# Kernel tuning notes

Measured on AMD Instinct MI355X. Metric: run time of the kernel, lower is better.

## Reference

```python
import jax, jax.numpy as jnp
import numpy as np

DROP_P = 0.5
DROP_KEY = jax.random.key(42)  # fixed key: deterministic dropout mask


def setup_inputs() -> dict:
    key = jax.random.key(0)
    k1, k2, k3 = jax.random.split(key, 3)
    B, H, S, D = 2, 16, 2048, 128
    x1 = jax.random.normal(k1, (B, H, S, D), dtype=jnp.float32)
    x2 = jax.random.normal(k2, (B, H, S, D), dtype=jnp.float32)
    # broadcastable per-head divisor; offset to keep it away from zero
    x3 = jax.random.uniform(k3, (B, H, 1, 1), dtype=jnp.float32) + 1.0
    return {"x1": x1, "x2": x2, "x3": x3}


def reference(x1, x2, x3):
    # v1 = x1 @ x2^T  -> [B,H,S,S]; v2 = v1 / x3 (broadcast divisor)
    scores = jnp.einsum('bhqd,bhkd->bhqk', x1, x2) / x3
    # v3 = softmax over last dim
    probs = jax.nn.softmax(scores, axis=-1)
    # v4 = dropout(p=0.5), training=True semantics: mask and rescale by 1/(1-p)
    keep = jax.random.bernoulli(DROP_KEY, 1.0 - DROP_P, probs.shape)
    probs = jnp.where(keep, probs / (1.0 - DROP_P), 0.0)
    # v5 = v4 @ x1 (note: values are x1, not a separate V); v6 = v5 + x2 residual
    out = jnp.einsum('bhqk,bhkd->bhqd', probs, x1) + x2
    return out
```

## Files before the change

### kernel.cpp

```cpp
#include <hip/hip_runtime.h>
#include <math.h>


constexpr int Sc = 2048, Dc = 128;
constexpr int BK = 64, NT = Sc / BK;
constexpr int KS_B = 16384, VS_B = 16384;
constexpr int PS_B = 8192;

typedef short bf16x8 __attribute__((ext_vector_type(8)));
typedef float f32x4 __attribute__((ext_vector_type(4)));
union U8 { uint4 u; bf16x8 v; };

__device__ __forceinline__ unsigned rotl32(unsigned x, int r) {
  return (x << r) | (x >> (32 - r));
}

__device__ __forceinline__ void tf2x32(unsigned x0, unsigned x1,
                                       unsigned &o0, unsigned &o1) {
  const unsigned ks0 = 0u, ks1 = 42u;
  const unsigned ks2 = 0x1BD11BDAu ^ 0u ^ 42u;
  x0 += ks0; x1 += ks1;
#define TFR(r) { x0 += x1; x1 = rotl32(x1, r); x1 ^= x0; }
  TFR(13) TFR(15) TFR(26) TFR(6)
  x0 += ks1; x1 += ks2 + 1u;
  TFR(17) TFR(29) TFR(16) TFR(24)
  x0 += ks2; x1 += ks0 + 2u;
  TFR(13) TFR(15) TFR(26) TFR(6)
  x0 += ks0; x1 += ks1 + 3u;
  TFR(17) TFR(29) TFR(16) TFR(24)
  x0 += ks1; x1 += ks2 + 4u;
  TFR(13) TFR(15) TFR(26) TFR(6)
  x0 += ks2; x1 += ks0 + 5u;
#undef TFR
  o0 = x0; o1 = x1;
}

__device__ __forceinline__ unsigned pk2rn(float a, float b) {
  return __builtin_amdgcn_perm(__float_as_uint(b) + 0x8000u,
                               __float_as_uint(a) + 0x8000u, 0x07060302u);
}

__device__ __forceinline__ void gload16(const void* g, void* l) {
  __builtin_amdgcn_global_load_lds(
      (const __attribute__((address_space(1))) void*)g,
      (__attribute__((address_space(3))) void*)l, 16, 0, 0);
}

__global__ __launch_bounds__(256)
void prepack(const float* __restrict__ x1, const float* __restrict__ x2,
             uint4* __restrict__ Kb, uint4* __restrict__ Vt) {
  __shared__ ushort Vl[64 * 68];
  const int tid = threadIdx.x, blk = blockIdx.x;
  const int half = blk & 1, tile = blk >> 1;
  const float* x2t = x2 + (size_t)tile * 8192;
  const float* x1t = x1 + (size_t)tile * 8192;
  uint4* KbT = Kb + (size_t)tile * 1024;
  uint4* VtT = Vt + (size_t)tile * 1024;
#pragma unroll
  for (int it = 0; it < 2; ++it) {
    int u = half * 512 + it * 256 + tid;
    int mt = u >> 8, c = (u >> 6) & 3, g = (u >> 4) & 3, m16 = u & 15;
    const float4* s = (const float4*)(x2t + (mt * 16 + m16) * 128 + c * 32 + g * 8);
    float4 f0 = s[0], f1 = s[1];
    KbT[u] = uint4{pk2rn(f0.x, f0.y), pk2rn(f0.z, f0.w),
                   pk2rn(f1.x, f1.y), pk2rn(f1.z, f1.w)};
  }
#pragma unroll
  for (int it = 0; it < 4; ++it) {
    int f = it * 256 + tid;
    int row = f >> 4, c4 = f & 15;
    float4 v = *(const float4*)(x1t + row * 128 + half * 64 + c4 * 4);
    *(uint2*)&Vl[row * 68 + c4 * 4] = uint2{pk2rn(v.x, v.y), pk2rn(v.z, v.w)};
  }
  __syncthreads();
#pragma unroll
  for (int it = 0; it < 2; ++it) {
    int ul = it * 256 + tid;
    int dtl = ul >> 7, c = (ul >> 6) & 1, g = (ul >> 4) & 3, m16 = ul & 15;
    int dl = dtl * 16 + m16, k0 = c * 32 + g * 8;
    unsigned w[4];
#pragma unroll
    for (int p = 0; p < 4; ++p) {
      unsigned lo = Vl[(k0 + 2 * p) * 68 + dl];
      unsigned hi = Vl[(k0 + 2 * p + 1) * 68 + dl];
      w[p] = lo | (hi << 16);
    }
    VtT[(((dtl + half * 4) * 2 + c) * 4 + g) * 16 + m16] = uint4{w[0], w[1], w[2], w[3]};
  }
}

__global__ __launch_bounds__(256, 4)
void attn4(const uint4* __restrict__ Kb, const uint4* __restrict__ Vt,
           const float* __restrict__ x1, const float* __restrict__ x2,
           const float* __restrict__ x3, float* __restrict__ out) {
  __shared__ uint4 smemv[(KS_B + VS_B + PS_B) / 16];
  char* smem = (char*)smemv;
  ushort* Ps = (ushort*)(smem + KS_B + VS_B);
  float* Os = (float*)smem;

  const int tid = threadIdx.x, wave = tid >> 6, lane = tid & 63;
  const int g = lane >> 4, q = lane & 15;
  const int blk = blockIdx.x, bh = blk & 31, qt = blk >> 5;

  const float* X1 = x1 + (size_t)bh * (Sc * Dc);
  const float* X2 = x2 + (size_t)bh * (Sc * Dc);
  float* outp = out + (size_t)bh * (Sc * Dc);
  const float cl2 = (1.0f / x3[bh]) * 1.4426950408889634f;

  const int qrow = qt * 64 + wave * 16 + q;
  const unsigned row_base = (unsigned)(bh * Sc + qrow) * (unsigned)Sc;

  bf16x8 qf[4];
  {
    const float4* qsrc = (const float4*)(X1 + (size_t)qrow * Dc);
#pragma unroll
    for (int c = 0; c < 4; ++c) {
      float4 f0 = qsrc[c * 8 + g * 2], f1 = qsrc[c * 8 + g * 2 + 1];
      U8 cv; cv.u = uint4{pk2rn(f0.x, f0.y), pk2rn(f0.z, f0.w),
                          pk2rn(f1.x, f1.y), pk2rn(f1.z, f1.w)};
      qf[c] = cv.v;
    }
  }

  f32x4 o[8];
#pragma unroll
  for (int i = 0; i < 8; ++i) o[i] = f32x4{0.f, 0.f, 0.f, 0.f};
  float l_run = 0.0f;
  const int tbase = bh * 32;
  ushort* pw = Ps + wave * 1024 + q * 64;

  for (int t = 0; t < NT; ++t) {
    __syncthreads();
    {
      const char* kg = (const char*)(Kb + (size_t)(tbase + t) * 1024);
      const char* vg = (const char*)(Vt + (size_t)(tbase + t) * 1024);
#pragma unroll
      for (int j = 0; j < 4; ++j) {
        int off = j * 4096 + wave * 1024 + lane * 16;
        gload16(kg + off, smem + off);
        gload16(vg + off, smem + KS_B + off);
      }
    }
    __syncthreads();

    f32x4 s0 = {}, s1 = {}, s2 = {}, s3 = {};
#pragma unroll
    for (int c = 0; c < 4; ++c) {
      U8 a0; a0.u = *(const uint4*)(smem + ((0 * 4 + c) * 64 + lane) * 16);
      U8 a1; a1.u = *(const uint4*)(smem + ((1 * 4 + c) * 64 + lane) * 16);
      U8 a2; a2.u = *(const uint4*)(smem + ((2 * 4 + c) * 64 + lane) * 16);
      U8 a3; a3.u = *(const uint4*)(smem + ((3 * 4 + c) * 64 + lane) * 16);
      s0 = __builtin_amdgcn_mfma_f32_16x16x32_bf16(a0.v, qf[c], s0, 0, 0, 0);
      s1 = __builtin_amdgcn_mfma_f32_16x16x32_bf16(a1.v, qf[c], s1, 0, 0, 0);
      s2 = __builtin_amdgcn_mfma_f32_16x16x32_bf16(a2.v, qf[c], s2, 0, 0, 0);
      s3 = __builtin_amdgcn_mfma_f32_16x16x32_bf16(a3.v, qf[c], s3, 0, 0, 0);
    }

    float pr[16];
    float ls = 0.0f;
#pragma unroll
    for (int i = 0; i < 4; ++i) { pr[i]      = __builtin_amdgcn_exp2f(s0[i] * cl2); ls += pr[i]; }
#pragma unroll
    for (int i = 0; i < 4; ++i) { pr[4 + i]  = __builtin_amdgcn_exp2f(s1[i] * cl2); ls += pr[4 + i]; }
#pragma unroll
    for (int i = 0; i < 4; ++i) { pr[8 + i]  = __builtin_amdgcn_exp2f(s2[i] * cl2); ls += pr[8 + i]; }
#pragma unroll
    for (int i = 0; i < 4; ++i) { pr[12 + i] = __builtin_amdgcn_exp2f(s3[i] * cl2); ls += pr[12 + i]; }
    ls += __shfl_xor(ls, 16);
    ls += __shfl_xor(ls, 32);
    l_run += ls;

    unsigned db = 0u;
    {
      const unsigned ib = row_base + (unsigned)(t * 64) + (unsigned)(g * 4);
#pragma unroll 4
      for (unsigned j = 0; j < 16; ++j) {
        unsigned key = ((j & 12u) << 2) | (j & 3u);
        unsigned a, b;
        tf2x32(0u, ib + key, a, b);
        db |= ((a ^ b) >> 31) << j;
      }
    }

#pragma unroll
    for (int mt = 0; mt < 4; ++mt) {
      float a0_ = ((db >> (mt * 4 + 0)) & 1u) ? 0.f : pr[mt * 4 + 0];
      float a1_ = ((db >> (mt * 4 + 1)) & 1u) ? 0.f : pr[mt * 4 + 1];
      float a2_ = ((db >> (mt * 4 + 2)) & 1u) ? 0.f : pr[mt * 4 + 2];
      float a3_ = ((db >> (mt * 4 + 3)) & 1u) ? 0.f : pr[mt * 4 + 3];
      *(uint2*)&pw[((mt * 4 + g) ^ q) * 4] = uint2{pk2rn(a0_, a1_), pk2rn(a2_, a3_)};
    }

#pragma unroll
    for (int c2 = 0; c2 < 2; ++c2) {
      int u0 = c2 * 8 + g * 2;
      uint2 b0 = *(const uint2*)&pw[(u0 ^ q) * 4];
      uint2 b1 = *(const uint2*)&pw[((u0 + 1) ^ q) * 4];
      U8 bfr; bfr.u = uint4{b0.x, b0.y, b1.x, b1.y};
#pragma unroll
      for (int dt = 0; dt < 8; ++dt) {
        U8 av; av.u = *(const uint4*)(smem + KS_B + ((dt * 2 + c2) * 64 + lane) * 16);
        o[dt] = __builtin_amdgcn_mfma_f32_16x16x32_bf16(av.v, bfr.v, o[dt], 0, 0, 0);
      }
    }
  }

  const float invl = 2.0f / l_run;
  __syncthreads();
  {
    float* ow = Os + (size_t)(wave * 16 + q) * 132;
#pragma unroll
    for (int dt = 0; dt < 8; ++dt) {
      int d = dt * 16 + g * 4;
      *(float4*)&ow[d] = float4{o[dt][0] * invl, o[dt][1] * invl,
                                o[dt][2] * invl, o[dt][3] * invl};
    }
  }
  __syncthreads();
#pragma unroll
  for (int it = 0; it < 8; ++it) {
    int f = it * 256 + tid;
    int ql = f >> 5, c4 = f & 31;
    float4 ov = *(const float4*)&Os[ql * 132 + c4 * 4];
    size_t goff = (size_t)(qt * 64 + ql) * Dc + c4 * 4;
    float4 xv = *(const float4*)&X2[goff];
    *(float4*)&outp[goff] = float4{ov.x + xv.x, ov.y + xv.y, ov.z + xv.z, ov.w + xv.w};
  }
}

extern "C" void kernel_launch(void* const* d_in, const int* in_sizes, int n_in,
                              void* d_out, int out_size, void* d_ws, size_t ws_size,
                              hipStream_t stream) {
  const float* x1 = (const float*)d_in[0];
  const float* x2 = (const float*)d_in[1];
  const float* x3 = (const float*)d_in[2];
  float* out = (float*)d_out;
  const size_t PREP = (size_t)1024 * 1024 * 16;
  uint4* Kb = (uint4*)d_ws;
  uint4* Vtg = (uint4*)((char*)d_ws + PREP);
  prepack<<<2048, 256, 0, stream>>>(x1, x2, Kb, Vtg);
  attn4<<<1024, 256, 0, stream>>>(Kb, Vtg, x1, x2, x3, out);
}
```

Before: 430.3 us.

## Double-buffer 32-key K/V tiles with async LDS prefetch and bitmask dropout

Halves the key tile from 64 to 32 and double-buffers K and V tiles in LDS. The next tile is prefetched with global_load_lds while the current tile is computed, which removes one barrier per iteration and overlaps the load with the MFMAs. Prepack is rewritten for the 32-key tile layout. Dropout is now applied by ANDing packed bf16 probabilities with per-element keep masks instead of per-bit selects, and the P buffer uses a padded stride in place of the XOR swizzle. The cost is twice as many loop iterations and barriers, plus a hand-written waitcnt immediate that must be correct for the loads to be visible.

```diff
diff --git a/kernel.cpp b/kernel.cpp
--- a/kernel.cpp
+++ b/kernel.cpp
@@ -3,9 +3,10 @@
 
 
 constexpr int Sc = 2048, Dc = 128;
-constexpr int BK = 64, NT = Sc / BK;
-constexpr int KS_B = 16384, VS_B = 16384;
-constexpr int PS_B = 8192;
+constexpr int BK = 32, NT = Sc / BK;
+constexpr int TILE_B = 8192;
+constexpr int PS_OFF = 32768;
+constexpr int PS_STRIDE = 80;
 
 typedef short bf16x8 __attribute__((ext_vector_type(8)));
 typedef float f32x4 __attribute__((ext_vector_type(4)));
@@ -35,9 +36,18 @@
   o0 = x0; o1 = x1;
 }
 
+__device__ __forceinline__ unsigned keepmask(unsigned idx) {
+  unsigned a, b; tf2x32(0u, idx, a, b);
+  return (unsigned)(((int)~(a ^ b)) >> 31);
+}
+
 __device__ __forceinline__ unsigned pk2rn(float a, float b) {
   return __builtin_amdgcn_perm(__float_as_uint(b) + 0x8000u,
                                __float_as_uint(a) + 0x8000u, 0x07060302u);
+}
+
+__device__ __forceinline__ unsigned hw2(unsigned ma, unsigned mb) {
+  return __builtin_amdgcn_perm(mb, ma, 0x05040100u);
 }
 
 __device__ __forceinline__ void gload16(const void* g, void* l) {
@@ -49,53 +59,52 @@
 __global__ __launch_bounds__(256)
 void prepack(const float* __restrict__ x1, const float* __restrict__ x2,
              uint4* __restrict__ Kb, uint4* __restrict__ Vt) {
-  __shared__ ushort Vl[64 * 68];
-  const int tid = threadIdx.x, blk = blockIdx.x;
-  const int half = blk & 1, tile = blk >> 1;
-  const float* x2t = x2 + (size_t)tile * 8192;
-  const float* x1t = x1 + (size_t)tile * 8192;
-  uint4* KbT = Kb + (size_t)tile * 1024;
-  uint4* VtT = Vt + (size_t)tile * 1024;
-#pragma unroll
-  for (int it = 0; it < 2; ++it) {
-    int u = half * 512 + it * 256 + tid;
-    int mt = u >> 8, c = (u >> 6) & 3, g = (u >> 4) & 3, m16 = u & 15;
-    const float4* s = (const float4*)(x2t + (mt * 16 + m16) * 128 + c * 32 + g * 8);
-    float4 f0 = s[0], f1 = s[1];
-    KbT[u] = uint4{pk2rn(f0.x, f0.y), pk2rn(f0.z, f0.w),
-                   pk2rn(f1.x, f1.y), pk2rn(f1.z, f1.w)};
-  }
+  __shared__ ushort Kl[32 * 136];
+  __shared__ ushort Vl[32 * 136];
+  const int tid = threadIdx.x;
+  const size_t tile = blockIdx.x;
+  const float4* ks = (const float4*)(x2 + tile * 4096);
+  const float4* vs = (const float4*)(x1 + tile * 4096);
 #pragma unroll
   for (int it = 0; it < 4; ++it) {
     int f = it * 256 + tid;
-    int row = f >> 4, c4 = f & 15;
-    float4 v = *(const float4*)(x1t + row * 128 + half * 64 + c4 * 4);
-    *(uint2*)&Vl[row * 68 + c4 * 4] = uint2{pk2rn(v.x, v.y), pk2rn(v.z, v.w)};
+    int row = f >> 5, c4 = f & 31;
+    float4 kv = ks[f];
+    float4 vv = vs[f];
+    *(uint2*)&Kl[row * 136 + c4 * 4] = uint2{pk2rn(kv.x, kv.y), pk2rn(kv.z, kv.w)};
+    *(uint2*)&Vl[row * 136 + c4 * 4] = uint2{pk2rn(vv.x, vv.y), pk2rn(vv.z, vv.w)};
   }
   __syncthreads();
 #pragma unroll
   for (int it = 0; it < 2; ++it) {
-    int ul = it * 256 + tid;
-    int dtl = ul >> 7, c = (ul >> 6) & 1, g = (ul >> 4) & 3, m16 = ul & 15;
-    int dl = dtl * 16 + m16, k0 = c * 32 + g * 8;
+    int u = it * 256 + tid;
+    int lane = u & 63, grp = u >> 6;
+    int mt = grp >> 2, c = grp & 3, m16 = lane & 15, g = lane >> 4;
+    uint4 w = *(const uint4*)&Kl[(mt * 16 + m16) * 136 + c * 32 + g * 8];
+    Kb[tile * 512 + u] = w;
+  }
+#pragma unroll
+  for (int it = 0; it < 2; ++it) {
+    int u = it * 256 + tid;
+    int lane = u & 63, dt = u >> 6, m16 = lane & 15, g = lane >> 4;
+    int d = dt * 16 + m16, k0 = g * 8;
     unsigned w[4];
 #pragma unroll
     for (int p = 0; p < 4; ++p) {
-      unsigned lo = Vl[(k0 + 2 * p) * 68 + dl];
-      unsigned hi = Vl[(k0 + 2 * p + 1) * 68 + dl];
+      unsigned lo = Vl[(k0 + 2 * p) * 136 + d];
+      unsigned hi = Vl[(k0 + 2 * p + 1) * 136 + d];
       w[p] = lo | (hi << 16);
     }
-    VtT[(((dtl + half * 4) * 2 + c) * 4 + g) * 16 + m16] = uint4{w[0], w[1], w[2], w[3]};
+    Vt[tile * 512 + u] = uint4{w[0], w[1], w[2], w[3]};
   }
 }
 
 __global__ __launch_bounds__(256, 4)
-void attn4(const uint4* __restrict__ Kb, const uint4* __restrict__ Vt,
+void attn5(const uint4* __restrict__ Kb, const uint4* __restrict__ Vt,
            const float* __restrict__ x1, const float* __restrict__ x2,
            const float* __restrict__ x3, float* __restrict__ out) {
-  __shared__ uint4 smemv[(KS_B + VS_B + PS_B) / 16];
+  __shared__ uint4 smemv[(PS_OFF + 5120) / 16];
   char* smem = (char*)smemv;
-  ushort* Ps = (ushort*)(smem + KS_B + VS_B);
   float* Os = (float*)smem;
 
   const int tid = threadIdx.x, wave = tid >> 6, lane = tid & 63;
@@ -126,86 +135,81 @@
 #pragma unroll
   for (int i = 0; i < 8; ++i) o[i] = f32x4{0.f, 0.f, 0.f, 0.f};
   float l_run = 0.0f;
-  const int tbase = bh * 32;
-  ushort* pw = Ps + wave * 1024 + q * 64;
+  const size_t tgbase = (size_t)bh * 64;
+  char* pwb = smem + PS_OFF + wave * 1280 + q * PS_STRIDE;
+
+  {
+    const char* kg = (const char*)(Kb + tgbase * 512);
+    const char* vg = (const char*)(Vt + tgbase * 512);
+#pragma unroll
+    for (int j = 0; j < 2; ++j) {
+      int off = j * 4096 + tid * 16;
+      gload16(kg + off, smem + off);
+      gload16(vg + off, smem + TILE_B + off);
+    }
+  }
 
   for (int t = 0; t < NT; ++t) {
+    const int b = t & 1;
+    char* cur = smem + b * (2 * TILE_B);
+    char* nxt = smem + (b ^ 1) * (2 * TILE_B);
+    __builtin_amdgcn_s_waitcnt(0x0F70);
     __syncthreads();
-    {
-      const char* kg = (const char*)(Kb + (size_t)(tbase + t) * 1024);
-      const char* vg = (const char*)(Vt + (size_t)(tbase + t) * 1024);
-#pragma unroll
-      for (int j = 0; j < 4; ++j) {
-        int off = j * 4096 + wave * 1024 + lane * 16;
-        gload16(kg + off, smem + off);
-        gload16(vg + off, smem + KS_B + off);
+    if (t + 1 < NT) {
+      const char* kg = (const char*)(Kb + (tgbase + t + 1) * 512);
+      const char* vg = (const char*)(Vt + (tgbase + t + 1) * 512);
+#pragma unroll
+      for (int j = 0; j < 2; ++j) {
+        int off = j * 4096 + tid * 16;
+        gload16(kg + off, nxt + off);
+        gload16(vg + off, nxt + TILE_B + off);
       }
     }
-    __syncthreads();
-
-    f32x4 s0 = {}, s1 = {}, s2 = {}, s3 = {};
+
+    f32x4 s0 = {}, s1 = {};
 #pragma unroll
     for (int c = 0; c < 4; ++c) {
-      U8 a0; a0.u = *(const uint4*)(smem + ((0 * 4 + c) * 64 + lane) * 16);
-      U8 a1; a1.u = *(const uint4*)(smem + ((1 * 4 + c) * 64 + lane) * 16);
-      U8 a2; a2.u = *(const uint4*)(smem + ((2 * 4 + c) * 64 + lane) * 16);
-      U8 a3; a3.u = *(const uint4*)(smem + ((3 * 4 + c) * 64 + lane) * 16);
+      U8 a0; a0.u = *(const uint4*)(cur + ((0 * 4 + c) * 64 + lane) * 16);
+      U8 a1; a1.u = *(const uint4*)(cur + ((1 * 4 + c) * 64 + lane) * 16);
       s0 = __builtin_amdgcn_mfma_f32_16x16x32_bf16(a0.v, qf[c], s0, 0, 0, 0);
       s1 = __builtin_amdgcn_mfma_f32_16x16x32_bf16(a1.v, qf[c], s1, 0, 0, 0);
-      s2 = __builtin_amdgcn_mfma_f32_16x16x32_bf16(a2.v, qf[c], s2, 0, 0, 0);
-      s3 = __builtin_amdgcn_mfma_f32_16x16x32_bf16(a3.v, qf[c], s3, 0, 0, 0);
-    }
-
-    float pr[16];
+    }
+
+    float pr[8];
     float ls = 0.0f;
 #pragma unroll
-    for (int i = 0; i < 4; ++i) { pr[i]      = __builtin_amdgcn_exp2f(s0[i] * cl2); ls += pr[i]; }
-#pragma unroll
-    for (int i = 0; i < 4; ++i) { pr[4 + i]  = __builtin_amdgcn_exp2f(s1[i] * cl2); ls += pr[4 + i]; }
-#pragma unroll
-    for (int i = 0; i < 4; ++i) { pr[8 + i]  = __builtin_amdgcn_exp2f(s2[i] * cl2); ls += pr[8 + i]; }
-#pragma unroll
-    for (int i = 0; i < 4; ++i) { pr[12 + i] = __builtin_amdgcn_exp2f(s3[i] * cl2); ls += pr[12 + i]; }
+    for (int i = 0; i < 4; ++i) { pr[i]     = __builtin_amdgcn_exp2f(s0[i] * cl2); ls += pr[i]; }
+#pragma unroll
+    for (int i = 0; i < 4; ++i) { pr[4 + i] = __builtin_amdgcn_exp2f(s1[i] * cl2); ls += pr[4 + i]; }
     ls += __shfl_xor(ls, 16);
     ls += __shfl_xor(ls, 32);
     l_run += ls;
 
-    unsigned db = 0u;
+    const unsigned ib = row_base + (unsigned)(t * 32) + (unsigned)(g * 4);
+    unsigned k00 = keepmask(ib + 0),  k01 = keepmask(ib + 1);
+    unsigned k02 = keepmask(ib + 2),  k03 = keepmask(ib + 3);
+    unsigned k10 = keepmask(ib + 16), k11 = keepmask(ib + 17);
+    unsigned k12 = keepmask(ib + 18), k13 = keepmask(ib + 19);
+
     {
-      const unsigned ib = row_base + (unsigned)(t * 64) + (unsigned)(g * 4);
-#pragma unroll 4
-      for (unsigned j = 0; j < 16; ++j) {
-        unsigned key = ((j & 12u) << 2) | (j & 3u);
-        unsigned a, b;
-        tf2x32(0u, ib + key, a, b);
-        db |= ((a ^ b) >> 31) << j;
-      }
-    }
-
-#pragma unroll
-    for (int mt = 0; mt < 4; ++mt) {
-      float a0_ = ((db >> (mt * 4 + 0)) & 1u) ? 0.f : pr[mt * 4 + 0];
-      float a1_ = ((db >> (mt * 4 + 1)) & 1u) ? 0.f : pr[mt * 4 + 1];
-      float a2_ = ((db >> (mt * 4 + 2)) & 1u) ? 0.f : pr[mt * 4 + 2];
-      float a3_ = ((db >> (mt * 4 + 3)) & 1u) ? 0.f : pr[mt * 4 + 3];
-      *(uint2*)&pw[((mt * 4 + g) ^ q) * 4] = uint2{pk2rn(a0_, a1_), pk2rn(a2_, a3_)};
-    }
-
-#pragma unroll
-    for (int c2 = 0; c2 < 2; ++c2) {
-      int u0 = c2 * 8 + g * 2;
-      uint2 b0 = *(const uint2*)&pw[(u0 ^ q) * 4];
-      uint2 b1 = *(const uint2*)&pw[((u0 + 1) ^ q) * 4];
-      U8 bfr; bfr.u = uint4{b0.x, b0.y, b1.x, b1.y};
-#pragma unroll
-      for (int dt = 0; dt < 8; ++dt) {
-        U8 av; av.u = *(const uint4*)(smem + KS_B + ((dt * 2 + c2) * 64 + lane) * 16);
-        o[dt] = __builtin_amdgcn_mfma_f32_16x16x32_bf16(av.v, bfr.v, o[dt], 0, 0, 0);
-      }
+      uint2 w0{pk2rn(pr[0], pr[1]) & hw2(k00, k01),
+               pk2rn(pr[2], pr[3]) & hw2(k02, k03)};
+      uint2 w1{pk2rn(pr[4], pr[5]) & hw2(k10, k11),
+               pk2rn(pr[6], pr[7]) & hw2(k12, k13)};
+      *(uint2*)(pwb + 0 * 32 + g * 8) = w0;
+      *(uint2*)(pwb + 1 * 32 + g * 8) = w1;
+    }
+
+    U8 bfr; bfr.u = *(const uint4*)(smem + PS_OFF + wave * 1280 + q * PS_STRIDE + g * 16);
+#pragma unroll
+    for (int dt = 0; dt < 8; ++dt) {
+      U8 av; av.u = *(const uint4*)(cur + TILE_B + (dt * 64 + lane) * 16);
+      o[dt] = __builtin_amdgcn_mfma_f32_16x16x32_bf16(av.v, bfr.v, o[dt], 0, 0, 0);
     }
   }
 
   const float invl = 2.0f / l_run;
+  __builtin_amdgcn_s_waitcnt(0x0F70);
   __syncthreads();
   {
     float* ow = Os + (size_t)(wave * 16 + q) * 132;
@@ -235,9 +239,9 @@
   const float* x2 = (const float*)d_in[1];
   const float* x3 = (const float*)d_in[2];
   float* out = (float*)d_out;
-  const size_t PREP = (size_t)1024 * 1024 * 16;
+  const size_t PREP = (size_t)2048 * 512 * 16;
   uint4* Kb = (uint4*)d_ws;
   uint4* Vtg = (uint4*)((char*)d_ws + PREP);
   prepack<<<2048, 256, 0, stream>>>(x1, x2, Kb, Vtg);
-  attn4<<<1024, 256, 0, stream>>>(Kb, Vtg, x1, x2, x3, out);
-}
+  attn5<<<1024, 256, 0, stream>>>(Kb, Vtg, x1, x2, x3, out);
+}
```

Result: slower. 485.0 us (+12.7%).
